# Performance work log

Measured on AMD Instinct MI355X. Metric: run time of the kernel, lower is better.

The kernel has to match this reference:

```python
import jax, jax.numpy as jnp
import numpy as np

B, C, D, H = 128, 8, 1024, 8
K_RANGE = (2, 3, 4, 5)


def setup_inputs() -> dict:
    key = jax.random.key(0)
    ks = jax.random.split(key, 10)
    s = 0.02
    return {
        "x": jax.random.normal(ks[0], (B, D), jnp.float32),
        # per-K prototype groups, shape (nb_classes, K, embed_dim) as in get_prototype_group()
        "p2": jax.random.normal(ks[1], (C, 2, D), jnp.float32),
        "p3": jax.random.normal(ks[2], (C, 3, D), jnp.float32),
        "p4": jax.random.normal(ks[3], (C, 4, D), jnp.float32),
        "p5": jax.random.normal(ks[4], (C, 5, D), jnp.float32),
        # per-class attention Block params (stacked over class axis)
        "ln_g": jnp.ones((C, D), jnp.float32),
        "ln_b": jnp.zeros((C, D), jnp.float32),
        "w_qkv": jax.random.normal(ks[5], (C, 3 * D, D), jnp.float32) * s,
        "b_qkv": jnp.zeros((C, 3 * D), jnp.float32),
        "w_proj": jax.random.normal(ks[6], (C, D, D), jnp.float32) * s,
        "b_proj": jnp.zeros((C, D), jnp.float32),
        # cls head
        "w_cls": jax.random.normal(ks[7], (C, D), jnp.float32) * s,
        "b_cls": jnp.zeros((C,), jnp.float32),
    }


def _proto_group(x, pg):
    """x: (B,D); pg: (C,K,D). Returns nearest proto (B,D), per-sample class group (B,K,D), class ids (B,)."""
    Cc, K, d = pg.shape
    flat = pg.reshape(Cc * K, d)
    # squared L2 distances (argmin identical to torch.cdist p=2 argmin)
    d2 = (jnp.sum(x * x, axis=1, keepdims=True)
          - 2.0 * (x @ flat.T)
          + jnp.sum(flat * flat, axis=1))
    idx = jnp.argmin(d2, axis=1)          # (B,)
    cls = idx // K                        # (B,)
    return flat[idx], pg[cls], cls


def _vicreg(x, nearest, proto_space, sim_c=25.0, std_c=25.0, cov_c=1.0):
    # sim: pull x toward its nearest prototype in every K-group
    repr_loss = jnp.mean((x[:, None, :] - nearest) ** 2)
    # std over batch of prototype space, unbiased var, eps=1e-4
    std = jnp.sqrt(jnp.var(proto_space, axis=0, ddof=1) + 1e-4)   # (S,D)
    std_loss = jnp.mean(jax.nn.relu(1.0 - std))
    # covariance of centered flattened prototype space
    ps = proto_space - jnp.mean(proto_space, axis=0)
    P = ps.reshape(-1, ps.shape[-1])                              # (B*S, D)
    cov = P.T @ P / (P.shape[0] - 1)
    cov_loss = ((cov ** 2).sum() - (jnp.diagonal(cov) ** 2).sum()) / ps.shape[-1]
    return sim_c * repr_loss + std_c * std_loss + cov_c * cov_loss


def _forward(x, p2, p3, p4, p5, ln_g, ln_b, w_qkv, b_qkv, w_proj, b_proj, w_cls, b_cls):
    groups = (p2, p3, p4, p5)
    nearest_list, space_list, cls = [], [], None
    for pg in groups:
        n, sp, cls = _proto_group(x, pg)   # cls kept from LAST group, as in torch code
        nearest_list.append(n)
        space_list.append(sp)
    nearest = jnp.stack(nearest_list, axis=1)     # (B, len(K_range), D)
    proto_space = jnp.concatenate(space_list, 1)  # (B, sum(K_range), D)

    vcr = _vicreg(x, nearest, proto_space)

    # per-class attention Block: LayerNorm -> MHA -> residual, vectorized over class axis c
    S = proto_space.shape[1]
    mu = proto_space.mean(-1, keepdims=True)
    var = proto_space.var(-1, keepdims=True)
    xn = (proto_space - mu) * jax.lax.rsqrt(var + 1e-5)               # (B,S,D)
    h = xn[None] * ln_g[:, None, None, :] + ln_b[:, None, None, :]    # (C,B,S,D)

    qkv = jnp.einsum('cbsd,cfd->cbsf', h, w_qkv) + b_qkv[:, None, None, :]
    dh = D // H
    qkv = qkv.reshape(C, B, S, 3, H, dh).transpose(3, 0, 1, 4, 2, 5)  # (3,C,B,H,S,dh)
    q, k, v = qkv[0] * (dh ** -0.5), qkv[1], qkv[2]
    attn = jax.nn.softmax(jnp.einsum('cbhqe,cbhke->cbhqk', q, k), axis=-1)
    o = jnp.einsum('cbhqk,cbhke->cbhqe', attn, v)                     # (C,B,H,S,dh)
    o = o.transpose(0, 1, 3, 2, 4).reshape(C, B, S, D)
    out = jnp.einsum('cbsd,ced->cbse', o, w_proj) + b_proj[:, None, None, :]
    attended = proto_space[None] + out                                # (C,B,S,D)

    # route each sample through the block of its (last-group) assigned class
    cond = attended[cls, jnp.arange(B)]                               # (B,S,D)
    cond = cond / jnp.maximum(jnp.linalg.norm(cond, axis=2, keepdims=True), 1e-12)
    pooled = cond.mean(1)                                             # (B,D)
    logits = pooled @ w_cls.T + b_cls
    return logits, vcr


def reference(x, p2, p3, p4, p5, ln_g, ln_b, w_qkv, b_qkv, w_proj, b_proj, w_cls, b_cls):
    return _forward(x, p2, p3, p4, p5, ln_g, ln_b, w_qkv, b_qkv, w_proj, b_proj, w_cls, b_cls)
```

## Files before the change

### kernel.cpp

```cpp
#include <hip/hip_runtime.h>
#include <math.h>

#define NB 128
#define ND 1024
#define NS 14
#define NDH 128

typedef float f32x4 __attribute__((ext_vector_type(4)));
typedef short bf16x8 __attribute__((ext_vector_type(8)));
typedef unsigned int u32x4 __attribute__((ext_vector_type(4)));

__device__ __forceinline__ unsigned short f2bf(float v) {
  unsigned int u = __builtin_bit_cast(unsigned int, v);
  return (unsigned short)((u + 0x7FFFu + ((u >> 16) & 1u)) >> 16);
}
__device__ __forceinline__ float bf2f(unsigned short u) {
  return __builtin_bit_cast(float, (unsigned int)u << 16);
}

__device__ __forceinline__ bf16x8 pack_bv(float4 w0, float4 w1) {
  unsigned int u0, u1, u2, u3;
  asm("v_cvt_pk_bf16_f32 %0, %1, %2" : "=v"(u0) : "v"(w0.x), "v"(w0.y));
  asm("v_cvt_pk_bf16_f32 %0, %1, %2" : "=v"(u1) : "v"(w0.z), "v"(w0.w));
  asm("v_cvt_pk_bf16_f32 %0, %1, %2" : "=v"(u2) : "v"(w1.x), "v"(w1.y));
  asm("v_cvt_pk_bf16_f32 %0, %1, %2" : "=v"(u3) : "v"(w1.z), "v"(w1.w));
  u32x4 u = {u0, u1, u2, u3};
  return __builtin_bit_cast(bf16x8, u);
}

__device__ __forceinline__ void s_decomp(int s, int& g, int& k) {
  if (s < 2)      { g = 0; k = s; }
  else if (s < 5) { g = 1; k = s - 2; }
  else if (s < 9) { g = 2; k = s - 5; }
  else            { g = 3; k = s - 9; }
}
__device__ __forceinline__ const float* grp_ptr(int g, const float* p2, const float* p3,
                                                const float* p4, const float* p5) {
  return g == 0 ? p2 : g == 1 ? p3 : g == 2 ? p4 : p5;
}
__device__ __forceinline__ int grp_base(int g) { return g == 0 ? 0 : g == 1 ? 16 : g == 2 ? 40 : 72; }
__device__ __forceinline__ int grp_k(int g) { return g + 2; }

__global__ __launch_bounds__(256) void k_ln_assign(
    const float* __restrict__ x,
    const float* __restrict__ p2, const float* __restrict__ p3,
    const float* __restrict__ p4, const float* __restrict__ p5,
    const float* __restrict__ ln_g, const float* __restrict__ ln_b,
    const float* __restrict__ w_proj, unsigned short* __restrict__ wpf,
    unsigned short* __restrict__ hbf2, float* __restrict__ pall,
    int* __restrict__ cls, int* __restrict__ rows_g, float* __restrict__ minv)
{
  int bid = blockIdx.x, t = threadIdx.x;
  if (bid >= 240) {
    int idxT = (bid - 240) * 256 + t;
    int c = idxT >> 17;
    int rem = idxT & 131071;
    int col = rem >> 7, kq = rem & 127;
    const float* src = w_proj + (((size_t)c * 1024 + col) << 10) + kq * 8;
    float4 w0 = *(const float4*)(src);
    float4 w1 = *(const float4*)(src + 4);
    bf16x8 v = pack_bv(w0, w1);
    size_t dst = ((((size_t)c * 64 + (col >> 4)) * 32 + (kq >> 2)) << 9)
               + ((kq & 3) * 16 + (col & 15)) * 8;
    *(bf16x8*)(wpf + dst) = v;
    return;
  }
  __shared__ __align__(16) float xs[ND];
  float4* xs4 = (float4*)xs;
  if (bid < 112) {
    int r = bid;
    const float* pp; int idx;
    if (r < 16)      { pp = p2; idx = r; }
    else if (r < 40) { pp = p3; idx = r - 16; }
    else if (r < 72) { pp = p4; idx = r - 40; }
    else             { pp = p5; idx = r - 72; }
    const float4* row4 = (const float4*)(pp + (size_t)idx * ND);
    float4 v = row4[t];
    xs4[t] = v;
    float s1 = v.x + v.y + v.z + v.w;
    float s2 = v.x * v.x + v.y * v.y + v.z * v.z + v.w * v.w;
    __shared__ float ra[256], rb[256];
    ra[t] = s1; rb[t] = s2; __syncthreads();
    for (int o = 128; o > 0; o >>= 1) { if (t < o) { ra[t] += ra[t + o]; rb[t] += rb[t + o]; } __syncthreads(); }
    __shared__ float mu, rstd;
    if (t == 0) {
      float m = ra[0] * (1.f / 1024.f);
      float var = rb[0] * (1.f / 1024.f) - m * m;
      mu = m; rstd = rsqrtf(var + 1e-5f);
    }
    __syncthreads();
    ((float4*)(pall + (size_t)r * ND))[t] = xs4[t];
    float4 xv = xs4[t];
    float nx = (xv.x - mu) * rstd, ny = (xv.y - mu) * rstd,
          nz = (xv.z - mu) * rstd, nw = (xv.w - mu) * rstd;
    int d0 = t * 4;
    int m = r >> 4, rr = r & 15;
    int kblk = d0 >> 5, qq = (d0 >> 3) & 3, e0 = d0 & 7;
    size_t fidx = (size_t)kblk * 3584 + m * 512 + (qq * 16 + rr) * 8 + e0;
#pragma unroll
    for (int c = 0; c < 8; ++c) {
      float4 g = ((const float4*)(ln_g + (size_t)c * ND))[t];
      float4 bb = ((const float4*)(ln_b + (size_t)c * ND))[t];
      ushort4 u;
      u.x = f2bf(nx * g.x + bb.x); u.y = f2bf(ny * g.y + bb.y);
      u.z = f2bf(nz * g.z + bb.z); u.w = f2bf(nw * g.w + bb.w);
      *(ushort4*)&hbf2[(size_t)c * 114688 + fidx] = u;
    }
  } else {
    int b = bid - 112;
    __shared__ float d2s[112];
    __shared__ int cls_s[4];
    const float4* xg4 = (const float4*)(x + (size_t)b * ND);
    xs4[t] = xg4[t];
    __syncthreads();
    int j = t >> 1, half = t & 1;
    if (j < 112) {
      const float* pp; int idx;
      if (j < 16)      { pp = p2; idx = j; }
      else if (j < 40) { pp = p3; idx = j - 16; }
      else if (j < 72) { pp = p4; idx = j - 40; }
      else             { pp = p5; idx = j - 72; }
      const float4* pr4 = (const float4*)(pp + (size_t)idx * ND);
      float acc = 0.f;
      int d0 = half * 128;
#pragma unroll 8
      for (int d = d0; d < d0 + 128; ++d) {
        float4 a = xs4[d], p = pr4[d];
        float dx = a.x - p.x, dy = a.y - p.y, dz = a.z - p.z, dw = a.w - p.w;
        acc += dx * dx + dy * dy + dz * dz + dw * dw;
      }
      acc += __shfl_xor(acc, 1, 2);
      if (half == 0) d2s[j] = acc;
    }
    __syncthreads();
    if (t < 4) {
      int base = grp_base(t), kg = grp_k(t), cnt = 8 * kg;
      float mv = d2s[base]; int mi = 0;
      for (int jj = 1; jj < cnt; ++jj) { float v = d2s[base + jj]; if (v < mv) { mv = v; mi = jj; } }
      int c = mi / kg;
      cls[b * 4 + t] = c; cls_s[t] = c;
      minv[b * 4 + t] = mv;
    }
    __syncthreads();
    if (t < NS) {
      int g, k; s_decomp(t, g, k);
      rows_g[b * NS + t] = grp_base(g) + cls_s[g] * grp_k(g) + k;
    }
  }
}

__global__ __launch_bounds__(256, 4) void k_qkv_prep(
    const unsigned short* __restrict__ hbf2, const float* __restrict__ w_qkv,
    const float* __restrict__ b_qkv, unsigned short* __restrict__ qkv_bf,
    const int* __restrict__ cls, const float* __restrict__ minv,
    int* __restrict__ counts, int* __restrict__ ccnt, int* __restrict__ order,
    int* __restrict__ posof, int* __restrict__ chunkidx, int* __restrict__ chunk_c,
    int* __restrict__ chunk_lo, int* __restrict__ chunkN, float* __restrict__ scal)
{
  int bid = blockIdx.x, t = threadIdx.x;
  if (bid == 0) {
    __shared__ int cnt_s[32];
    __shared__ int cc_s[8];
    __shared__ float red[128];
    if (t < 32) cnt_s[t] = 0;
    if (t < 8) cc_s[t] = 0;
    if (t < 4) scal[t] = 0.f;
    __syncthreads();
    if (t < 128) {
      int c3;
#pragma unroll
      for (int g = 0; g < 4; ++g) {
        int c = cls[t * 4 + g];
        atomicAdd(&cnt_s[g * 8 + c], 1);
        if (g == 3) c3 = c;
      }
      int pos = atomicAdd(&cc_s[c3], 1);
      order[c3 * 128 + pos] = t;
      posof[t] = pos;
      red[t] = minv[t * 4 + 0] + minv[t * 4 + 1] + minv[t * 4 + 2] + minv[t * 4 + 3];
    }
    __syncthreads();
    for (int o = 64; o > 0; o >>= 1) { if (t < o) red[t] += red[t + o]; __syncthreads(); }
    if (t == 0) {
      scal[0] = red[0];
      int T = 0;
      for (int c = 0; c < 8; ++c) {
        chunkidx[c] = T;
        int nch = (cc_s[c] + 15) >> 4;
        for (int j = 0; j < nch; ++j) { chunk_c[T] = c; chunk_lo[T] = j * 16; ++T; }
      }
      chunkN[0] = T;
    }
    if (t < 32) counts[t] = cnt_s[t];
    if (t < 8) ccnt[t] = cc_s[t];
    return;
  }
  __shared__ __align__(16) float lred[3 * 14 * 256];
  int qb = bid - 1;
  int c = qb / 96, xb = qb - c * 96;
  int lane = t & 63, ks = t >> 6;
  int r16 = lane & 15, q = lane >> 4;
  int col0 = xb * 32 + r16, col1 = col0 + 16;
  const float* Wp0 = w_qkv + ((size_t)c * 3072 + col0) * ND + ks * 256 + q * 8;
  const float* Wp1 = Wp0 + (size_t)16 * ND;
  const unsigned short* Hp = hbf2 + (size_t)c * 114688 + (size_t)(ks * 8) * 3584 + lane * 8;
  f32x4 acc0[7] = {}, acc1[7] = {};
#pragma unroll
  for (int i = 0; i < 8; ++i) {
    float4 w00 = *(const float4*)(Wp0 + i * 32);
    float4 w01 = *(const float4*)(Wp0 + i * 32 + 4);
    float4 w10 = *(const float4*)(Wp1 + i * 32);
    float4 w11 = *(const float4*)(Wp1 + i * 32 + 4);
    bf16x8 av[7];
#pragma unroll
    for (int m = 0; m < 7; ++m) av[m] = *(const bf16x8*)(Hp + (size_t)i * 3584 + m * 512);
    bf16x8 bv0 = pack_bv(w00, w01);
    bf16x8 bv1 = pack_bv(w10, w11);
#pragma unroll
    for (int m = 0; m < 7; ++m) {
      acc0[m] = __builtin_amdgcn_mfma_f32_16x16x32_bf16(av[m], bv0, acc0[m], 0, 0, 0);
      acc1[m] = __builtin_amdgcn_mfma_f32_16x16x32_bf16(av[m], bv1, acc1[m], 0, 0, 0);
    }
  }
  if (ks) {
#pragma unroll
    for (int m = 0; m < 7; ++m) {
      *(f32x4*)&lred[((ks - 1) * 14 + m) * 256 + lane * 4] = acc0[m];
      *(f32x4*)&lred[((ks - 1) * 14 + 7 + m) * 256 + lane * 4] = acc1[m];
    }
  }
  __syncthreads();
  if (ks == 0) {
    float bq0 = b_qkv[(size_t)c * 3072 + col0];
    float bq1 = b_qkv[(size_t)c * 3072 + col1];
#pragma unroll
    for (int m = 0; m < 7; ++m) {
      f32x4 s0 = acc0[m], s1 = acc1[m];
#pragma unroll
      for (int sk = 0; sk < 3; ++sk) {
        s0 += *(const f32x4*)&lred[(sk * 14 + m) * 256 + lane * 4];
        s1 += *(const f32x4*)&lred[(sk * 14 + 7 + m) * 256 + lane * 4];
      }
#pragma unroll
      for (int r = 0; r < 4; ++r) {
        int row = m * 16 + q * 4 + r;
        qkv_bf[((size_t)c * 112 + row) * 3072 + col0] = f2bf(s0[r] + bq0);
        qkv_bf[((size_t)c * 112 + row) * 3072 + col1] = f2bf(s1[r] + bq1);
      }
    }
  }
}

__global__ __launch_bounds__(256) void k_attn_stats(
    const unsigned short* __restrict__ qkv_bf, const int* __restrict__ cls,
    const int* __restrict__ rows_g, const int* __restrict__ posof,
    const int* __restrict__ chunkidx, unsigned short* __restrict__ obf2,
    const float* __restrict__ p2, const float* __restrict__ p3,
    const float* __restrict__ p4, const float* __restrict__ p5,
    const int* __restrict__ counts, float* __restrict__ M, float* __restrict__ scal)
{
  int bid = blockIdx.x, t = threadIdx.x;
  if (bid < 1024) {
    __shared__ __align__(16) float qs[NS * NDH], ks2[NS * NDH], vs[NS * NDH];
    __shared__ float sc[NS * NS];
    __shared__ int rg[NS];
    int h = bid & 7, b = bid >> 3;
    if (t < NS) rg[t] = rows_g[b * NS + t];
    __syncthreads();
    int cp = cls[b * 4 + 3];
    int pos = posof[b];
    size_t gbase = (size_t)(chunkidx[cp] + (pos >> 4)) * 229376;
    int slot = pos & 15;
    const float scale = 0.08838834764831843f;
    for (int i = t; i < NS * 32; i += 256) {
      int s = i >> 5, e4 = (i & 31) * 4;
      size_t base = ((size_t)cp * 112 + rg[s]) * 3072 + h * NDH + e4;
      ushort4 uq = *(const ushort4*)&qkv_bf[base];
      ushort4 uk = *(const ushort4*)&qkv_bf[base + 1024];
      ushort4 uv = *(const ushort4*)&qkv_bf[base + 2048];
      int o = s * NDH + e4;
      qs[o]     = bf2f(uq.x) * scale; qs[o + 1] = bf2f(uq.y) * scale;
      qs[o + 2] = bf2f(uq.z) * scale; qs[o + 3] = bf2f(uq.w) * scale;
      ks2[o]     = bf2f(uk.x); ks2[o + 1] = bf2f(uk.y);
      ks2[o + 2] = bf2f(uk.z); ks2[o + 3] = bf2f(uk.w);
      vs[o]     = bf2f(uv.x); vs[o + 1] = bf2f(uv.y);
      vs[o + 2] = bf2f(uv.z); vs[o + 3] = bf2f(uv.w);
    }
    __syncthreads();
    if (t < NS * NS) {
      int si = t / NS, sj = t - (t / NS) * NS;
      const float4* qa = (const float4*)&qs[si * NDH];
      const float4* kb = (const float4*)&ks2[sj * NDH];
      float acc = 0.f;
#pragma unroll 8
      for (int e4 = 0; e4 < 32; ++e4) {
        float4 a = qa[e4], k4 = kb[e4];
        acc += a.x * k4.x + a.y * k4.y + a.z * k4.z + a.w * k4.w;
      }
      sc[t] = acc;
    }
    __syncthreads();
    if (t < NS) {
      float mx = -1e30f;
      for (int j = 0; j < NS; ++j) mx = fmaxf(mx, sc[t * NS + j]);
      float e_[NS]; float sum = 0.f;
      for (int j = 0; j < NS; ++j) { float e = expf(sc[t * NS + j] - mx); e_[j] = e; sum += e; }
      float inv = 1.f / sum;
      for (int j = 0; j < NS; ++j) sc[t * NS + j] = e_[j] * inv;
    }
    __syncthreads();
    for (int i = t; i < NS * 32; i += 256) {
      int s = i >> 5, e4 = i & 31;
      float4 a = {0.f, 0.f, 0.f, 0.f};
#pragma unroll
      for (int j = 0; j < NS; ++j) {
        float w = sc[s * NS + j];
        float4 v4 = ((const float4*)&vs[j * NDH])[e4];
        a.x += w * v4.x; a.y += w * v4.y; a.z += w * v4.z; a.w += w * v4.w;
      }
      int row = slot * 14 + s;
      int m = row >> 4, r16 = row & 15;
      int d0 = h * NDH + e4 * 4;
      int kblk = d0 >> 5, qq = (d0 >> 3) & 3, e0 = d0 & 7;
      ushort4 u; u.x = f2bf(a.x); u.y = f2bf(a.y); u.z = f2bf(a.z); u.w = f2bf(a.w);
      *(ushort4*)&obf2[gbase + (size_t)kblk * 7168 + m * 512 + (qq * 16 + r16) * 8 + e0] = u;
    }
  } else {
    int idx = (bid - 1024) * 256 + t;
    int s = idx >> 10, d = idx & 1023;
    int g, k; s_decomp(s, g, k);
    const float* pp = grp_ptr(g, p2, p3, p4, p5);
    int kg = grp_k(g);
    float vc[8], nc[8];
    float sum = 0.f, sumsq = 0.f;
#pragma unroll
    for (int c = 0; c < 8; ++c) {
      float v = pp[((size_t)(c * kg + k)) * ND + d];
      float n = (float)counts[g * 8 + c];
      vc[c] = v; nc[c] = n;
      sum += n * v; sumsq += n * v * v;
    }
    float mean = sum * (1.f / 128.f);
    float var = (sumsq - 128.f * mean * mean) * (1.f / 127.f);
    float sd = sqrtf(var + 1e-4f);
#pragma unroll
    for (int c = 0; c < 8; ++c)
      M[((size_t)(s * 8 + c)) * ND + d] = sqrtf(nc[c] * (1.f / 1791.f)) * (vc[c] - mean);
    float part = fmaxf(1.f - sd, 0.f);
    __shared__ float red[256];
    red[t] = part; __syncthreads();
    for (int o = 128; o > 0; o >>= 1) { if (t < o) red[t] += red[t + o]; __syncthreads(); }
    if (t == 0) atomicAdd(&scal[1], red[0]);
  }
}

__global__ __launch_bounds__(512) void k_proj_gram(
    const unsigned short* __restrict__ obf2, const unsigned short* __restrict__ wpf,
    const int* __restrict__ order,
    const int* __restrict__ ccnt, const int* __restrict__ chunk_c,
    const int* __restrict__ chunk_lo, const int* __restrict__ chunkN,
    const int* __restrict__ rows_g,
    const float* __restrict__ b_proj,
    const float* __restrict__ pall, float* __restrict__ att,
    const float* __restrict__ M, float* __restrict__ scal)
{
  int bid = blockIdx.x, t = threadIdx.x;
  if (bid < 960) {
    int g = bid / 64, xb = bid - g * 64;
    if (g >= chunkN[0]) return;
    __shared__ __align__(16) float lred[3 * 2 * 7 * 256];
    __shared__ int sid_s[16];
    int c = chunk_c[g], lo = chunk_lo[g];
    int cnt = ccnt[c];
    int nb = cnt - lo; if (nb > 16) nb = 16;
    int lane = t & 63, wid = t >> 6;
    int rh = wid & 1, ks = wid >> 1;
    if (t < 16) sid_s[t] = order[c * 128 + lo + ((t < nb) ? t : nb - 1)];
    int r16 = lane & 15, q = lane >> 4;
    int col = xb * 16 + r16;
    const unsigned short* Wf = wpf + ((((size_t)c * 64 + xb) * 32 + ks * 8) << 9) + lane * 8;
    const unsigned short* Ap = obf2 + (size_t)g * 229376 + (size_t)(ks * 8) * 7168 + rh * 3584 + lane * 8;
    f32x4 acc[7] = {};
#pragma unroll
    for (int i = 0; i < 8; ++i) {
      bf16x8 bv = *(const bf16x8*)(Wf + (size_t)i * 512);
      const unsigned short* ak = Ap + (size_t)i * 7168;
#pragma unroll
      for (int m = 0; m < 7; ++m) {
        bf16x8 av = *(const bf16x8*)(ak + m * 512);
        acc[m] = __builtin_amdgcn_mfma_f32_16x16x32_bf16(av, bv, acc[m], 0, 0, 0);
      }
    }
    if (ks) {
#pragma unroll
      for (int m = 0; m < 7; ++m)
        *(f32x4*)&lred[(((ks - 1) * 2 + rh) * 7 + m) * 256 + lane * 4] = acc[m];
    }
    __syncthreads();
    if (ks == 0) {
      float bp = b_proj[(size_t)c * ND + col];
#pragma unroll
      for (int m = 0; m < 7; ++m) {
        f32x4 a1 = *(const f32x4*)&lred[((0 * 2 + rh) * 7 + m) * 256 + lane * 4];
        f32x4 a2 = *(const f32x4*)&lred[((1 * 2 + rh) * 7 + m) * 256 + lane * 4];
        f32x4 a3 = *(const f32x4*)&lred[((2 * 2 + rh) * 7 + m) * 256 + lane * 4];
#pragma unroll
        for (int r = 0; r < 4; ++r) {
          int row = rh * 112 + m * 16 + q * 4 + r;
          int slot = row / 14, s = row - slot * 14;
          if (slot < nb) {
            int b = sid_s[slot];
            float res = pall[(size_t)rows_g[b * NS + s] * ND + col];
            att[((size_t)b * NS + s) * ND + col] = acc[m][r] + a1[r] + a2[r] + a3[r] + bp + res;
          }
        }
      }
    }
  } else if (bid < 1072) {
    int r = bid - 960;
    __shared__ __align__(16) float mi[ND];
    __shared__ float red2[128];
    float4* mi4 = (float4*)mi;
    const float4* src4 = (const float4*)(M + (size_t)r * ND);
    if (t < 256) mi4[t] = src4[t];
    if (t < 128) red2[t] = 0.f;
    __syncthreads();
    int j = t >> 2, qd = t & 3;
    float p = 0.f;
    if (j < 112) {
      const float4* mj4 = (const float4*)(M + (size_t)j * ND);
      float acc = 0.f;
#pragma unroll 8
      for (int d = qd * 64; d < qd * 64 + 64; ++d) {
        float4 a = mi4[d], b = mj4[d];
        acc += a.x * b.x + a.y * b.y + a.z * b.z + a.w * b.w;
      }
      acc += __shfl_xor(acc, 1, 4);
      acc += __shfl_xor(acc, 2, 4);
      p = acc * acc;
    }
    if (qd == 0 && j < 112) red2[j] = p;
    __syncthreads();
    for (int o = 64; o > 0; o >>= 1) { if (t < o) red2[t] += red2[t + o]; __syncthreads(); }
    if (t == 0) atomicAdd(&scal[2], red2[0]);
  } else {
    int d = (bid - 1072) * 512 + t;
    float tsum = 0.f;
    for (int r = 0; r < 112; ++r) { float v = M[(size_t)r * ND + d]; tsum += v * v; }
    __shared__ float red3[512];
    red3[t] = tsum * tsum; __syncthreads();
    for (int o = 256; o > 0; o >>= 1) { if (t < o) red3[t] += red3[t + o]; __syncthreads(); }
    if (t == 0) atomicAdd(&scal[3], red3[0]);
  }
}

__global__ __launch_bounds__(256) void k_final(
    const float* __restrict__ att, const float* __restrict__ w_cls,
    const float* __restrict__ b_cls, const float* __restrict__ scal,
    float* __restrict__ out)
{
  int b = blockIdx.x, t = threadIdx.x;
  __shared__ __align__(16) float as[NS * ND];
  __shared__ float wred[NS][4];
  __shared__ float inv[NS];
  __shared__ __align__(16) float pooled[ND];
  int lane = t & 63, w = t >> 6;
#pragma unroll
  for (int s = 0; s < NS; ++s) {
    float4 v = ((const float4*)(att + ((size_t)b * NS + s) * ND))[t];
    ((float4*)&as[s * ND])[t] = v;
    float p = v.x * v.x + v.y * v.y + v.z * v.z + v.w * v.w;
#pragma unroll
    for (int o = 32; o > 0; o >>= 1) p += __shfl_xor(p, o, 64);
    if (lane == 0) wred[s][w] = p;
  }
  __syncthreads();
  if (t < NS) {
    float s2 = wred[t][0] + wred[t][1] + wred[t][2] + wred[t][3];
    inv[t] = 1.f / fmaxf(sqrtf(s2), 1e-12f);
  }
  __syncthreads();
  float4 pa = {0.f, 0.f, 0.f, 0.f};
#pragma unroll
  for (int s = 0; s < NS; ++s) {
    float iv = inv[s];
    float4 v = ((const float4*)&as[s * ND])[t];
    pa.x += iv * v.x; pa.y += iv * v.y; pa.z += iv * v.z; pa.w += iv * v.w;
  }
  const float k14 = 1.f / 14.f;
  pa.x *= k14; pa.y *= k14; pa.z *= k14; pa.w *= k14;
  ((float4*)pooled)[t] = pa;
  __syncthreads();
  int c = t >> 5, l = t & 31;
  float acc = 0.f;
#pragma unroll
  for (int k = 0; k < 8; ++k) {
    int i4 = l + k * 32;
    float4 p4 = ((const float4*)pooled)[i4];
    float4 wc = ((const float4*)(w_cls + (size_t)c * ND))[i4];
    acc += p4.x * wc.x + p4.y * wc.y + p4.z * wc.z + p4.w * wc.w;
  }
  for (int o = 16; o > 0; o >>= 1) acc += __shfl_down(acc, o, 32);
  if (l == 0) out[b * 8 + c] = acc + b_cls[c];
  if (b == 0 && t == 0) {
    float repr = scal[0] * (1.f / (128.f * 4.f * 1024.f));
    float stdl = scal[1] * (1.f / 14336.f);
    float covl = (scal[2] - scal[3]) * (1.f / 1024.f);
    out[1024] = 25.f * repr + 25.f * stdl + covl;
  }
}

extern "C" void kernel_launch(void* const* d_in, const int* in_sizes, int n_in,
                              void* d_out, int out_size, void* d_ws, size_t ws_size,
                              hipStream_t stream) {
  const float* x      = (const float*)d_in[0];
  const float* p2     = (const float*)d_in[1];
  const float* p3     = (const float*)d_in[2];
  const float* p4     = (const float*)d_in[3];
  const float* p5     = (const float*)d_in[4];
  const float* ln_g   = (const float*)d_in[5];
  const float* ln_b   = (const float*)d_in[6];
  const float* w_qkv  = (const float*)d_in[7];
  const float* b_qkv  = (const float*)d_in[8];
  const float* w_proj = (const float*)d_in[9];
  const float* b_proj = (const float*)d_in[10];
  const float* w_cls  = (const float*)d_in[11];
  const float* b_cls  = (const float*)d_in[12];
  float* out = (float*)d_out;
  char* ws = (char*)d_ws;

  float* scal      = (float*)(ws + 0);
  int*   counts    = (int*)(ws + 64);
  int*   ccnt      = (int*)(ws + 192);
  int*   cls       = (int*)(ws + 256);
  int*   rows_g    = (int*)(ws + 2304);
  int*   order     = (int*)(ws + 9472);
  float* minv      = (float*)(ws + 13568);
  int*   posof     = (int*)(ws + 15616);
  int*   chunkidx  = (int*)(ws + 16128);
  int*   chunk_c   = (int*)(ws + 16160);
  int*   chunk_lo  = (int*)(ws + 16224);
  int*   chunkN    = (int*)(ws + 16288);
  float* pall      = (float*)(ws + 16384);
  unsigned short* hbf2 = (unsigned short*)(ws + 475136);
  unsigned short* qkvb = (unsigned short*)(ws + 2310144);
  unsigned short* obf2 = (unsigned short*)(ws + 7815168);
  float* att       = (float*)(ws + 15155200);
  float* M         = (float*)(ws + 22495232);
  unsigned short* wpf = (unsigned short*)(ws + 22953984);

  k_ln_assign<<<4336, 256, 0, stream>>>(x, p2, p3, p4, p5, ln_g, ln_b, w_proj, wpf,
                                        hbf2, pall, cls, rows_g, minv);
  k_qkv_prep<<<769, 256, 0, stream>>>(hbf2, w_qkv, b_qkv, qkvb, cls, minv,
                                      counts, ccnt, order, posof, chunkidx, chunk_c, chunk_lo, chunkN, scal);
  k_attn_stats<<<1080, 256, 0, stream>>>(qkvb, cls, rows_g, posof, chunkidx, obf2,
                                         p2, p3, p4, p5, counts, M, scal);
  k_proj_gram<<<1074, 512, 0, stream>>>(obf2, wpf, order, ccnt, chunk_c, chunk_lo, chunkN, rows_g,
                                        b_proj, pall, att, M, scal);
  k_final<<<128, 256, 0, stream>>>(att, w_cls, b_cls, scal, out);
}
```

Measured before the change: 120.5 us.

## Halve QKV tile width and stage weights via swizzled LDS

```diff
diff --git a/kernel.cpp b/kernel.cpp
--- a/kernel.cpp
+++ b/kernel.cpp
@@ -157,6 +157,7 @@
     int* __restrict__ posof, int* __restrict__ chunkidx, int* __restrict__ chunk_c,
     int* __restrict__ chunk_lo, int* __restrict__ chunkN, float* __restrict__ scal)
 {
+  __shared__ __align__(16) char smem[32768];
   int bid = blockIdx.x, t = threadIdx.x;
   if (bid == 0) {
     __shared__ int cnt_s[32];
@@ -195,57 +196,63 @@
     if (t < 8) ccnt[t] = cc_s[t];
     return;
   }
-  __shared__ __align__(16) float lred[3 * 14 * 256];
   int qb = bid - 1;
-  int c = qb / 96, xb = qb - c * 96;
+  int c = qb / 192, xb = qb - c * 192;
+  int col0 = xb * 16;
+  unsigned short* Wl = (unsigned short*)smem;
+  {
+    const float* Wbase = w_qkv + ((size_t)c * 3072 + col0) * ND;
+    int k0 = t * 4;
+    int ksq = t >> 6, kblk = (t >> 3) & 7, qq = (t >> 1) & 3, e0 = (t & 1) * 4;
+    int sw = ((kblk & 3) << 2) + qq;
+    int ebase = ((ksq * 8 + kblk) * 64 + qq * 16) * 8 + e0;
+#pragma unroll
+    for (int j = 0; j < 16; ++j) {
+      float4 w = *(const float4*)(Wbase + (size_t)j * ND + k0);
+      unsigned int u0, u1;
+      asm("v_cvt_pk_bf16_f32 %0, %1, %2" : "=v"(u0) : "v"(w.x), "v"(w.y));
+      asm("v_cvt_pk_bf16_f32 %0, %1, %2" : "=v"(u1) : "v"(w.z), "v"(w.w));
+      unsigned int* dst = (unsigned int*)&Wl[ebase + (j ^ sw) * 8];
+      dst[0] = u0; dst[1] = u1;
+    }
+  }
+  __syncthreads();
   int lane = t & 63, ks = t >> 6;
   int r16 = lane & 15, q = lane >> 4;
-  int col0 = xb * 32 + r16, col1 = col0 + 16;
-  const float* Wp0 = w_qkv + ((size_t)c * 3072 + col0) * ND + ks * 256 + q * 8;
-  const float* Wp1 = Wp0 + (size_t)16 * ND;
   const unsigned short* Hp = hbf2 + (size_t)c * 114688 + (size_t)(ks * 8) * 3584 + lane * 8;
-  f32x4 acc0[7] = {}, acc1[7] = {};
+  f32x4 acc[7] = {};
 #pragma unroll
   for (int i = 0; i < 8; ++i) {
-    float4 w00 = *(const float4*)(Wp0 + i * 32);
-    float4 w01 = *(const float4*)(Wp0 + i * 32 + 4);
-    float4 w10 = *(const float4*)(Wp1 + i * 32);
-    float4 w11 = *(const float4*)(Wp1 + i * 32 + 4);
-    bf16x8 av[7];
-#pragma unroll
-    for (int m = 0; m < 7; ++m) av[m] = *(const bf16x8*)(Hp + (size_t)i * 3584 + m * 512);
-    bf16x8 bv0 = pack_bv(w00, w01);
-    bf16x8 bv1 = pack_bv(w10, w11);
+    int sr = ((i & 3) << 2) + q;
+    bf16x8 bv = *(const bf16x8*)&Wl[(((ks * 8 + i) * 64) + q * 16 + (r16 ^ sr)) * 8];
+    const unsigned short* hk = Hp + (size_t)i * 3584;
 #pragma unroll
     for (int m = 0; m < 7; ++m) {
-      acc0[m] = __builtin_amdgcn_mfma_f32_16x16x32_bf16(av[m], bv0, acc0[m], 0, 0, 0);
-      acc1[m] = __builtin_amdgcn_mfma_f32_16x16x32_bf16(av[m], bv1, acc1[m], 0, 0, 0);
-    }
-  }
+      bf16x8 av = *(const bf16x8*)(hk + m * 512);
+      acc[m] = __builtin_amdgcn_mfma_f32_16x16x32_bf16(av, bv, acc[m], 0, 0, 0);
+    }
+  }
+  __syncthreads();
+  float* lred = (float*)smem;
   if (ks) {
 #pragma unroll
-    for (int m = 0; m < 7; ++m) {
-      *(f32x4*)&lred[((ks - 1) * 14 + m) * 256 + lane * 4] = acc0[m];
-      *(f32x4*)&lred[((ks - 1) * 14 + 7 + m) * 256 + lane * 4] = acc1[m];
-    }
+    for (int m = 0; m < 7; ++m)
+      *(f32x4*)&lred[((ks - 1) * 7 + m) * 256 + lane * 4] = acc[m];
   }
   __syncthreads();
   if (ks == 0) {
-    float bq0 = b_qkv[(size_t)c * 3072 + col0];
-    float bq1 = b_qkv[(size_t)c * 3072 + col1];
+    int col = col0 + r16;
+    float bq = b_qkv[(size_t)c * 3072 + col];
 #pragma unroll
     for (int m = 0; m < 7; ++m) {
-      f32x4 s0 = acc0[m], s1 = acc1[m];
-#pragma unroll
-      for (int sk = 0; sk < 3; ++sk) {
-        s0 += *(const f32x4*)&lred[(sk * 14 + m) * 256 + lane * 4];
-        s1 += *(const f32x4*)&lred[(sk * 14 + 7 + m) * 256 + lane * 4];
-      }
+      f32x4 s0 = acc[m];
+#pragma unroll
+      for (int sk = 0; sk < 3; ++sk)
+        s0 += *(const f32x4*)&lred[(sk * 7 + m) * 256 + lane * 4];
 #pragma unroll
       for (int r = 0; r < 4; ++r) {
         int row = m * 16 + q * 4 + r;
-        qkv_bf[((size_t)c * 112 + row) * 3072 + col0] = f2bf(s0[r] + bq0);
-        qkv_bf[((size_t)c * 112 + row) * 3072 + col1] = f2bf(s1[r] + bq1);
+        qkv_bf[((size_t)c * 112 + row) * 3072 + col] = f2bf(s0[r] + bq);
       }
     }
   }
@@ -551,8 +558,8 @@
 
   k_ln_assign<<<4336, 256, 0, stream>>>(x, p2, p3, p4, p5, ln_g, ln_b, w_proj, wpf,
                                         hbf2, pall, cls, rows_g, minv);
-  k_qkv_prep<<<769, 256, 0, stream>>>(hbf2, w_qkv, b_qkv, qkvb, cls, minv,
-                                      counts, ccnt, order, posof, chunkidx, chunk_c, chunk_lo, chunkN, scal);
+  k_qkv_prep<<<1537, 256, 0, stream>>>(hbf2, w_qkv, b_qkv, qkvb, cls, minv,
+                                       counts, ccnt, order, posof, chunkidx, chunk_c, chunk_lo, chunkN, scal);
   k_attn_stats<<<1080, 256, 0, stream>>>(qkvb, cls, rows_g, posof, chunkidx, obf2,
                                          p2, p3, p4, p5, counts, M, scal);
   k_proj_gram<<<1074, 512, 0, stream>>>(obf2, wpf, order, ccnt, chunk_c, chunk_lo, chunkN, rows_g,
```

Measured after the change: 124.8 us. +3.5%, slower.

## Move w_proj bf16 repack into qkv kernel with LDS-staged coalesced writes

Applied to the files above, without the earlier changes.

```diff
diff --git a/kernel.cpp b/kernel.cpp
--- a/kernel.cpp
+++ b/kernel.cpp
@@ -46,25 +46,10 @@
     const float* __restrict__ p2, const float* __restrict__ p3,
     const float* __restrict__ p4, const float* __restrict__ p5,
     const float* __restrict__ ln_g, const float* __restrict__ ln_b,
-    const float* __restrict__ w_proj, unsigned short* __restrict__ wpf,
     unsigned short* __restrict__ hbf2, float* __restrict__ pall,
     int* __restrict__ cls, int* __restrict__ rows_g, float* __restrict__ minv)
 {
   int bid = blockIdx.x, t = threadIdx.x;
-  if (bid >= 240) {
-    int idxT = (bid - 240) * 256 + t;
-    int c = idxT >> 17;
-    int rem = idxT & 131071;
-    int col = rem >> 7, kq = rem & 127;
-    const float* src = w_proj + (((size_t)c * 1024 + col) << 10) + kq * 8;
-    float4 w0 = *(const float4*)(src);
-    float4 w1 = *(const float4*)(src + 4);
-    bf16x8 v = pack_bv(w0, w1);
-    size_t dst = ((((size_t)c * 64 + (col >> 4)) * 32 + (kq >> 2)) << 9)
-               + ((kq & 3) * 16 + (col & 15)) * 8;
-    *(bf16x8*)(wpf + dst) = v;
-    return;
-  }
   __shared__ __align__(16) float xs[ND];
   float4* xs4 = (float4*)xs;
   if (bid < 112) {
@@ -152,11 +137,13 @@
 __global__ __launch_bounds__(256, 4) void k_qkv_prep(
     const unsigned short* __restrict__ hbf2, const float* __restrict__ w_qkv,
     const float* __restrict__ b_qkv, unsigned short* __restrict__ qkv_bf,
+    const float* __restrict__ w_proj, unsigned short* __restrict__ wpf,
     const int* __restrict__ cls, const float* __restrict__ minv,
     int* __restrict__ counts, int* __restrict__ ccnt, int* __restrict__ order,
     int* __restrict__ posof, int* __restrict__ chunkidx, int* __restrict__ chunk_c,
     int* __restrict__ chunk_lo, int* __restrict__ chunkN, float* __restrict__ scal)
 {
+  __shared__ __align__(16) float lred[3 * 14 * 256];
   int bid = blockIdx.x, t = threadIdx.x;
   if (bid == 0) {
     __shared__ int cnt_s[32];
@@ -195,8 +182,33 @@
     if (t < 8) ccnt[t] = cc_s[t];
     return;
   }
-  __shared__ __align__(16) float lred[3 * 14 * 256];
-  int qb = bid - 1;
+  int u = bid - 1, grp = u / 7, rem = u - grp * 7;
+  if (rem >= 3) {
+    int i = grp * 4 + (rem - 3);
+    int c = i >> 7, r2 = i & 127, cb = r2 >> 1, kb2 = r2 & 1;
+    unsigned short* tl2 = (unsigned short*)lred;
+    const float* Wb = w_proj + (((size_t)c * 1024 + cb * 16) << 10) + kb2 * 512;
+    int r = t >> 4, kk = (t & 15) * 8, g = t & 15;
+    float4 a0[4], a1[4];
+#pragma unroll
+    for (int j = 0; j < 4; ++j) {
+      a0[j] = *(const float4*)(Wb + (size_t)r * ND + j * 128 + kk);
+      a1[j] = *(const float4*)(Wb + (size_t)r * ND + j * 128 + kk + 4);
+    }
+#pragma unroll
+    for (int j = 0; j < 4; ++j) {
+      bf16x8 v = pack_bv(a0[j], a1[j]);
+      *(bf16x8*)&tl2[j * 2048 + (g * 16 + (r ^ g)) * 8] = v;
+    }
+    __syncthreads();
+    size_t B = ((size_t)((c * 64 + cb) * 32 + kb2 * 16)) << 9;
+    int gr = t >> 4, rr = t & 15;
+#pragma unroll
+    for (int j = 0; j < 4; ++j)
+      *(bf16x8*)&wpf[B + j * 2048 + t * 8] = *(const bf16x8*)&tl2[j * 2048 + (gr * 16 + (rr ^ gr)) * 8];
+    return;
+  }
+  int qb = grp * 3 + rem;
   int c = qb / 96, xb = qb - c * 96;
   int lane = t & 63, ks = t >> 6;
   int r16 = lane & 15, q = lane >> 4;
@@ -549,10 +561,10 @@
   float* M         = (float*)(ws + 22495232);
   unsigned short* wpf = (unsigned short*)(ws + 22953984);
 
-  k_ln_assign<<<4336, 256, 0, stream>>>(x, p2, p3, p4, p5, ln_g, ln_b, w_proj, wpf,
-                                        hbf2, pall, cls, rows_g, minv);
-  k_qkv_prep<<<769, 256, 0, stream>>>(hbf2, w_qkv, b_qkv, qkvb, cls, minv,
-                                      counts, ccnt, order, posof, chunkidx, chunk_c, chunk_lo, chunkN, scal);
+  k_ln_assign<<<240, 256, 0, stream>>>(x, p2, p3, p4, p5, ln_g, ln_b,
+                                       hbf2, pall, cls, rows_g, minv);
+  k_qkv_prep<<<1793, 256, 0, stream>>>(hbf2, w_qkv, b_qkv, qkvb, w_proj, wpf, cls, minv,
+                                       counts, ccnt, order, posof, chunkidx, chunk_c, chunk_lo, chunkN, scal);
   k_attn_stats<<<1080, 256, 0, stream>>>(qkvb, cls, rows_g, posof, chunkidx, obf2,
                                          p2, p3, p4, p5, counts, M, scal);
   k_proj_gram<<<1074, 512, 0, stream>>>(obf2, wpf, order, ccnt, chunk_c, chunk_lo, chunkN, rows_g,
```

After: 120.3 us. Within noise of the previous version (-0.2%).
